# Kernel optimization log

Measured on AMD Instinct MI355X. Metric: run time of the kernel, lower is better.

The kernel has to match this reference:

```python
import jax, jax.numpy as jnp
import numpy as np

N = 10000      # nodes
E = 160000     # edges (avg degree 16)
D = 128        # channels
H = 4          # heads
C = 128        # per-head dim (PyG: out_channels per head = channels)
HC = H * C
EPS_SOFTMAX = 1e-16
EPS_NORM = 1e-5


def setup_inputs() -> dict:
    key = jax.random.key(0)
    ks = jax.random.split(key, 12)
    s = 1.0 / np.sqrt(D)
    sb = 1.0 / np.sqrt(3 * D)
    return {
        "x": jax.random.normal(ks[0], (N, D), jnp.float32),
        "edge_index": jax.random.randint(ks[1], (2, E), 0, N, dtype=jnp.int64),
        "Wq": jax.random.normal(ks[2], (D, HC), jnp.float32) * s,
        "bq": jnp.zeros((HC,), jnp.float32),
        "Wk": jax.random.normal(ks[3], (D, HC), jnp.float32) * s,
        "bk": jnp.zeros((HC,), jnp.float32),
        "Wv": jax.random.normal(ks[4], (D, HC), jnp.float32) * s,
        "bv": jnp.zeros((HC,), jnp.float32),
        "Wskip": jax.random.normal(ks[5], (D, D), jnp.float32) * s,
        "bskip": jnp.zeros((D,), jnp.float32),
        "Wbeta": jax.random.normal(ks[6], (3 * D,), jnp.float32) * sb,  # lin_beta, bias=False
        "gn_weight": jnp.ones((D,), jnp.float32),
        "gn_bias": jnp.zeros((D,), jnp.float32),
        "gn_mean_scale": jnp.ones((D,), jnp.float32),
    }


def reference(x, edge_index, Wq, bq, Wk, bk, Wv, bv, Wskip, bskip, Wbeta,
              gn_weight, gn_bias, gn_mean_scale):
    n = x.shape[0]
    src, dst = edge_index[0], edge_index[1]  # messages flow src(j) -> dst(i)

    # Projections [N,H,C]
    q = (x @ Wq + bq).reshape(n, H, C)
    k = (x @ Wk + bk).reshape(n, H, C)
    v = (x @ Wv + bv).reshape(n, H, C)

    # Per-edge attention logits [E,H]
    alpha = jnp.einsum('ehc,ehc->eh', q[dst], k[src]) / jnp.sqrt(jnp.float32(C))

    # Segment softmax over incoming edges of each dst node
    amax = jax.ops.segment_max(alpha, dst, num_segments=n)       # [N,H]
    amax = jnp.where(jnp.isfinite(amax), amax, 0.0)
    ex = jnp.exp(alpha - amax[dst])                              # [E,H]
    denom = jax.ops.segment_sum(ex, dst, num_segments=n)         # [N,H]
    attn = ex / (denom[dst] + EPS_SOFTMAX)                       # [E,H]

    # Weighted scatter-aggregate, then mean over heads (concat=False)
    msgs = attn[:, :, None] * v[src]                             # [E,H,C]
    out = jax.ops.segment_sum(msgs, dst, num_segments=n)         # [N,H,C]
    out = out.mean(axis=1)                                       # [N,D]

    # Beta-gated skip (PyG: beta = sigmoid(lin_beta([out, x_r, out - x_r])))
    skip = x @ Wskip + bskip
    beta = jax.nn.sigmoid(jnp.concatenate([out, skip, out - skip], axis=-1) @ Wbeta)
    beta = beta[:, None]
    out = beta * skip + (1.0 - beta) * out

    # GraphNorm (single graph): (x - mean_scale*mean) / sqrt(var + eps) * w + b
    mean = out.mean(axis=0)
    centered = out - gn_mean_scale * mean
    var = (centered * centered).mean(axis=0)
    out = gn_weight * centered / jnp.sqrt(var + EPS_NORM) + gn_bias

    # GELU (exact) + residual (shapes match); dropout is identity in eval
    out = jax.nn.gelu(out, approximate=False)
    return out + x
```

## Files before the change

kernel.cpp:

```cpp
#include <hip/hip_runtime.h>
#include <hip/hip_bf16.h>
#include <math.h>

#define D_DIM 128
#define HC_DIM 512
#define CAP 128

typedef __attribute__((ext_vector_type(8))) short bf16x8;
typedef __attribute__((ext_vector_type(4))) float f32x4;
typedef __attribute__((ext_vector_type(2))) float f32x2;
typedef __attribute__((ext_vector_type(2))) _Float16 h16x2;

static __device__ __forceinline__ unsigned short f2bf(float f) {
  unsigned u = __float_as_uint(f);
  unsigned r = (u + 0x7fffu + ((u >> 16) & 1u)) >> 16;
  return (unsigned short)r;
}
static __device__ __forceinline__ float bflo(unsigned u) {
  return __uint_as_float(u << 16);
}
static __device__ __forceinline__ float bfhi(unsigned u) {
  return __uint_as_float(u & 0xffff0000u);
}

__global__ void prep_kernel(const float* __restrict__ x,
                            const float* __restrict__ Wq, const float* __restrict__ Wk,
                            const float* __restrict__ Wv, const float* __restrict__ Wskip,
                            const float* __restrict__ bq, const float* __restrict__ bk,
                            const float* __restrict__ bv, const float* __restrict__ bskip,
                            unsigned short* __restrict__ xb,
                            unsigned short* __restrict__ wcat,
                            float* __restrict__ bcat,
                            int* __restrict__ zbase, int zwords, int N) {
  int t = blockIdx.x * 256 + threadIdx.x;
  int X4 = N * 32;
  if (t < X4) {
    float4 f = *(const float4*)&x[t * 4];
    ushort4 o;
    o.x = f2bf(f.x); o.y = f2bf(f.y); o.z = f2bf(f.z); o.w = f2bf(f.w);
    *(ushort4*)&xb[t * 4] = o;
  } else if (t < X4 + 1664 * 128) {
    int widx = t - X4;
    if (widx < 3 * 65536) {
      int segi = widx >> 16;
      int r = widx & 65535;
      int kk = r >> 9;
      int m = r & 511;
      const float* W = (segi == 0) ? Wq : (segi == 1) ? Wk : Wv;
      wcat[(size_t)(segi * 512 + m) * 128 + kk] = f2bf(W[kk * 512 + m]);
    } else {
      int r = widx - 3 * 65536;
      int kk = r >> 7;
      int m = r & 127;
      wcat[(size_t)(1536 + m) * 128 + kk] = f2bf(Wskip[kk * 128 + m]);
    }
  } else if (t < X4 + 1664 * 128 + 1664) {
    int b = t - X4 - 1664 * 128;
    bcat[b] = (b < 512) ? bq[b] : (b < 1024) ? bk[b - 512]
            : (b < 1536) ? bv[b - 1024] : bskip[b - 1536];
  } else if (t < X4 + 1664 * 128 + 1664 + zwords) {
    zbase[t - X4 - 1664 * 128 - 1664] = 0;
  }
}

__global__ __launch_bounds__(256) void gemm_mfma_kernel(
    const unsigned short* __restrict__ Xb, const unsigned short* __restrict__ Wt,
    const float* __restrict__ bcat, unsigned short* __restrict__ qb,
    unsigned short* __restrict__ kf, unsigned char* __restrict__ v8,
    float* __restrict__ skip,
    const int* __restrict__ src, const int* __restrict__ dst,
    int* __restrict__ cnt, int* __restrict__ bsrc, int N, int E) {
  const int tid = threadIdx.x;
  {
    int nblk = gridDim.x * gridDim.y;
    int lb = blockIdx.y * gridDim.x + blockIdx.x;
    int per = (E + nblk - 1) / nblk;
    int e0 = lb * per;
    int e1 = min(e0 + per, E);
    for (int e = e0 + tid; e < e1; e += 256) {
      int d = dst[e];
      int p = atomicAdd(&cnt[d], 1);
      if (p < CAP) bsrc[d * CAP + p] = src[e];
    }
  }
  const int wave = tid >> 6, lane = tid & 63;
  const int l16 = lane & 15, quad = lane >> 4;
  const int row0 = (blockIdx.x * 4 + wave) * 64;
  const int col0 = blockIdx.y * 64;

  const unsigned short* xrow[4];
#pragma unroll
  for (int i = 0; i < 4; ++i) {
    int r = row0 + i * 16 + l16;
    if (r >= N) r = N - 1;
    xrow[i] = Xb + (size_t)r * 128;
  }
  const unsigned short* wrow[4];
  float bias[4];
#pragma unroll
  for (int j = 0; j < 4; ++j) {
    int c = col0 + j * 16 + l16;
    wrow[j] = Wt + (size_t)c * 128;
    bias[j] = bcat[c];
  }

  f32x4 acc[4][4] = {};
#pragma unroll
  for (int kk = 0; kk < 4; ++kk) {
    int k0 = kk * 32 + quad * 8;
    bf16x8 a[4], b[4];
#pragma unroll
    for (int i = 0; i < 4; ++i) a[i] = *(const bf16x8*)(xrow[i] + k0);
#pragma unroll
    for (int j = 0; j < 4; ++j) b[j] = *(const bf16x8*)(wrow[j] + k0);
#pragma unroll
    for (int i = 0; i < 4; ++i)
#pragma unroll
      for (int j = 0; j < 4; ++j)
        acc[i][j] = __builtin_amdgcn_mfma_f32_16x16x32_bf16(a[i], b[j], acc[i][j], 0, 0, 0);
  }

  const int kind = (col0 < 512) ? 0 : (col0 < 1024) ? 1 : (col0 < 1536) ? 2 : 3;
#pragma unroll
  for (int i = 0; i < 4; ++i) {
#pragma unroll
    for (int reg = 0; reg < 4; ++reg) {
      int r = row0 + i * 16 + quad * 4 + reg;
      if (r < N) {
#pragma unroll
        for (int j = 0; j < 4; ++j) {
          int cidx = col0 + j * 16 + l16;
          float val = acc[i][j][reg] + bias[j];
          if (kind == 0) {
            qb[(size_t)r * 512 + cidx] = f2bf(val);
          } else if (kind == 1) {
            _Float16 hv = (_Float16)val;
            kf[(size_t)r * 512 + cidx - 512] = *(unsigned short*)&hv;
          } else if (kind == 2) {
            int pk = __builtin_amdgcn_cvt_pk_fp8_f32(val, val, 0, false);
            v8[(size_t)r * 512 + cidx - 1024] = (unsigned char)pk;
          } else {
            skip[(size_t)r * 128 + cidx - 1536] = val;
          }
        }
      }
    }
  }
}

__global__ __launch_bounds__(256) void attn_kernel(
    const unsigned short* __restrict__ qb, const unsigned short* __restrict__ kf,
    const unsigned char* __restrict__ v8, const int* __restrict__ cnt,
    const int* __restrict__ bsrc, unsigned* __restrict__ oh, int N, int nper) {
  int bx = blockIdx.x;
  int head = bx / nper;
  int tid = threadIdx.x;
  int w = tid >> 6, lane = tid & 63;
  int node = (bx - head * nper) * 4 + w;
  if (node >= N) return;
  int g = lane >> 4, j = lane & 15;

  const float qscale = 0.08838834764831845f * 1.4426950408889634f;
  int4 qi = *(const int4*)(qb + (size_t)node * 512 + head * 128 + j * 8);
  h16x2 qh0, qh1, qh2, qh3;
  qh0[0] = (_Float16)(bflo(qi.x) * qscale); qh0[1] = (_Float16)(bfhi(qi.x) * qscale);
  qh1[0] = (_Float16)(bflo(qi.y) * qscale); qh1[1] = (_Float16)(bfhi(qi.y) * qscale);
  qh2[0] = (_Float16)(bflo(qi.z) * qscale); qh2[1] = (_Float16)(bfhi(qi.z) * qscale);
  qh3[0] = (_Float16)(bflo(qi.w) * qscale); qh3[1] = (_Float16)(bfhi(qi.w) * qscale);

  const unsigned short* kb = kf + head * 128 + j * 8;
  const unsigned char* vb = v8 + head * 128 + j * 8;
  int count = min(cnt[node], CAP);
  const int* bp = bsrc + node * CAP;
  float lsum = 0.f;
  float o0 = 0.f, o1 = 0.f, o2 = 0.f, o3 = 0.f;
  float o4 = 0.f, o5 = 0.f, o6 = 0.f, o7 = 0.f;

  if (count > 0) {
    int e = bp[(g < count) ? g : 0];
    uint4 kw = *(const uint4*)(kb + (size_t)e * 512);
    uint2 vw = *(const uint2*)(vb + (size_t)e * 512);
    for (int idx = 0; idx < count; idx += 4) {
      int rem = count - idx;
      int nrem = rem - 4;
      int en = (nrem > 0) ? bp[idx + 4 + ((g < nrem) ? g : 0)] : e;
      uint4 kwn = *(const uint4*)(kb + (size_t)en * 512);
      uint2 vwn = *(const uint2*)(vb + (size_t)en * 512);
      float p = __builtin_amdgcn_fdot2(qh0, *(h16x2*)&kw.x, 0.f, false);
      p = __builtin_amdgcn_fdot2(qh1, *(h16x2*)&kw.y, p, false);
      p = __builtin_amdgcn_fdot2(qh2, *(h16x2*)&kw.z, p, false);
      p = __builtin_amdgcn_fdot2(qh3, *(h16x2*)&kw.w, p, false);
      p += __shfl_xor(p, 1);
      p += __shfl_xor(p, 2);
      p += __shfl_xor(p, 4);
      p += __shfl_xor(p, 8);
      float a = (g < rem) ? p : -1e30f;
      float wgt = exp2f(a);
      f32x2 v01 = __builtin_amdgcn_cvt_pk_f32_fp8(vw.x, false);
      f32x2 v23 = __builtin_amdgcn_cvt_pk_f32_fp8(vw.x, true);
      f32x2 v45 = __builtin_amdgcn_cvt_pk_f32_fp8(vw.y, false);
      f32x2 v67 = __builtin_amdgcn_cvt_pk_f32_fp8(vw.y, true);
      lsum += wgt;
      o0 += wgt * v01.x; o1 += wgt * v01.y;
      o2 += wgt * v23.x; o3 += wgt * v23.y;
      o4 += wgt * v45.x; o5 += wgt * v45.y;
      o6 += wgt * v67.x; o7 += wgt * v67.y;
      kw = kwn; vw = vwn; e = en;
    }
  }
  o0 += __shfl_xor(o0, 16); o0 += __shfl_xor(o0, 32);
  o1 += __shfl_xor(o1, 16); o1 += __shfl_xor(o1, 32);
  o2 += __shfl_xor(o2, 16); o2 += __shfl_xor(o2, 32);
  o3 += __shfl_xor(o3, 16); o3 += __shfl_xor(o3, 32);
  o4 += __shfl_xor(o4, 16); o4 += __shfl_xor(o4, 32);
  o5 += __shfl_xor(o5, 16); o5 += __shfl_xor(o5, 32);
  o6 += __shfl_xor(o6, 16); o6 += __shfl_xor(o6, 32);
  o7 += __shfl_xor(o7, 16); o7 += __shfl_xor(o7, 32);
  lsum += __shfl_xor(lsum, 16); lsum += __shfl_xor(lsum, 32);
  float inv = 1.f / (lsum + 1e-16f);
  if (g == 0) {
    unsigned d0 = (unsigned)f2bf(o0 * inv) | ((unsigned)f2bf(o1 * inv) << 16);
    unsigned d1 = (unsigned)f2bf(o2 * inv) | ((unsigned)f2bf(o3 * inv) << 16);
    unsigned d2 = (unsigned)f2bf(o4 * inv) | ((unsigned)f2bf(o5 * inv) << 16);
    unsigned d3 = (unsigned)f2bf(o6 * inv) | ((unsigned)f2bf(o7 * inv) << 16);
    int4 st; st.x = (int)d0; st.y = (int)d1; st.z = (int)d2; st.w = (int)d3;
    *(int4*)(oh + ((size_t)head * N + node) * 64 + j * 4) = st;
  }
}

__global__ __launch_bounds__(256) void combine_kernel(
    const unsigned* __restrict__ oh, const float* __restrict__ skip,
    const float* __restrict__ Wbeta, float* __restrict__ out2,
    float* __restrict__ colsum, float* __restrict__ colsq, int N) {
  int tid = threadIdx.x;
  int lane = tid & 63, w = tid >> 6;
  int wid = blockIdx.x * 4 + w;
  float2 wb0 = *(const float2*)&Wbeta[lane * 2];
  float2 wb1 = *(const float2*)&Wbeta[128 + lane * 2];
  float2 wb2 = *(const float2*)&Wbeta[256 + lane * 2];
  float cs0 = 0.f, cq0 = 0.f, cs1 = 0.f, cq1 = 0.f;
#pragma unroll
  for (int k = 0; k < 4; ++k) {
    int n = wid + k * 2500;
    if (n < N) {
      unsigned h0 = oh[((size_t)0 * N + n) * 64 + lane];
      unsigned h1 = oh[((size_t)1 * N + n) * 64 + lane];
      unsigned h2 = oh[((size_t)2 * N + n) * 64 + lane];
      unsigned h3 = oh[((size_t)3 * N + n) * 64 + lane];
      float a0 = 0.25f * (bflo(h0) + bflo(h1) + bflo(h2) + bflo(h3));
      float a1 = 0.25f * (bfhi(h0) + bfhi(h1) + bfhi(h2) + bfhi(h3));
      float2 s = *(const float2*)&skip[(size_t)n * 128 + lane * 2];
      float p = a0 * wb0.x + s.x * wb1.x + (a0 - s.x) * wb2.x +
                a1 * wb0.y + s.y * wb1.y + (a1 - s.y) * wb2.y;
#pragma unroll
      for (int dmask = 1; dmask < 64; dmask <<= 1) p += __shfl_xor(p, dmask);
      float beta = 1.f / (1.f + __expf(-p));
      float o0 = beta * s.x + (1.f - beta) * a0;
      float o1 = beta * s.y + (1.f - beta) * a1;
      float2 ov; ov.x = o0; ov.y = o1;
      *(float2*)&out2[(size_t)n * 128 + lane * 2] = ov;
      cs0 += o0; cq0 += o0 * o0;
      cs1 += o1; cq1 += o1 * o1;
    }
  }
  __shared__ float red[4][128];
  __shared__ float redq[4][128];
  red[w][lane * 2] = cs0;
  red[w][lane * 2 + 1] = cs1;
  redq[w][lane * 2] = cq0;
  redq[w][lane * 2 + 1] = cq1;
  __syncthreads();
  if (w == 0) {
    int c = lane * 2;
    float s0 = red[0][c] + red[1][c] + red[2][c] + red[3][c];
    float s1 = red[0][c + 1] + red[1][c + 1] + red[2][c + 1] + red[3][c + 1];
    float q0 = redq[0][c] + redq[1][c] + redq[2][c] + redq[3][c];
    float q1 = redq[0][c + 1] + redq[1][c + 1] + redq[2][c + 1] + redq[3][c + 1];
    atomicAdd(&colsum[c], s0);
    atomicAdd(&colsum[c + 1], s1);
    atomicAdd(&colsq[c], q0);
    atomicAdd(&colsq[c + 1], q1);
  }
}

__global__ void final_kernel(const float* __restrict__ out2,
                             const float* __restrict__ colsum,
                             const float* __restrict__ colsq,
                             const float* __restrict__ gnw,
                             const float* __restrict__ gnb,
                             const float* __restrict__ gnms,
                             const float* __restrict__ x,
                             float* __restrict__ y, int total2, float invN) {
  int i = blockIdx.x * 256 + threadIdx.x;
  if (i < total2) {
    int c = (i & 63) * 2;
    float2 cs = *(const float2*)&colsum[c];
    float2 cq = *(const float2*)&colsq[c];
    float2 gw = *(const float2*)&gnw[c];
    float2 gb = *(const float2*)&gnb[c];
    float2 gs = *(const float2*)&gnms[c];
    float mean0 = cs.x * invN, mean1 = cs.y * invN;
    float var0 = cq.x * invN - mean0 * mean0 * gs.x * (2.f - gs.x);
    float var1 = cq.y * invN - mean1 * mean1 * gs.y * (2.f - gs.y);
    float mul0 = gw.x / sqrtf(var0 + 1e-5f);
    float mul1 = gw.y / sqrtf(var1 + 1e-5f);
    float2 o = *(const float2*)&out2[i * 2];
    float2 xx = *(const float2*)&x[i * 2];
    float t0 = (o.x - gs.x * mean0) * mul0 + gb.x;
    float t1 = (o.y - gs.y * mean1) * mul1 + gb.y;
    float g0 = 0.5f * t0 * (1.f + erff(t0 * 0.70710678118654752f));
    float g1 = 0.5f * t1 * (1.f + erff(t1 * 0.70710678118654752f));
    float2 r; r.x = g0 + xx.x; r.y = g1 + xx.y;
    *(float2*)&y[i * 2] = r;
  }
}

extern "C" void kernel_launch(void* const* d_in, const int* in_sizes, int n_in,
                              void* d_out, int out_size, void* d_ws, size_t ws_size,
                              hipStream_t stream) {
  const float* x     = (const float*)d_in[0];
  const int*   ei    = (const int*)d_in[1];
  const float* Wq    = (const float*)d_in[2];
  const float* bq    = (const float*)d_in[3];
  const float* Wk    = (const float*)d_in[4];
  const float* bk    = (const float*)d_in[5];
  const float* Wv    = (const float*)d_in[6];
  const float* bv    = (const float*)d_in[7];
  const float* Wskip = (const float*)d_in[8];
  const float* bskip = (const float*)d_in[9];
  const float* Wbeta = (const float*)d_in[10];
  const float* gnw   = (const float*)d_in[11];
  const float* gnb   = (const float*)d_in[12];
  const float* gnms  = (const float*)d_in[13];

  const int N = in_sizes[0] / D_DIM;
  const int E = in_sizes[1] / 2;
  const int* src = ei;
  const int* dst = ei + E;

  char* p = (char*)d_ws;
  unsigned short* qb = (unsigned short*)p; p += (size_t)N * 512 * 2;
  unsigned short* kf = (unsigned short*)p; p += (size_t)N * 512 * 2;
  unsigned char*  v8 = (unsigned char*)p;  p += (size_t)N * 512;
  unsigned*       oh = (unsigned*)p;       p += (size_t)4 * N * 64 * 4;
  float*          skip = (float*)p;        p += (size_t)N * 128 * 4;
  float*          out2 = (float*)p;        p += (size_t)N * 128 * 4;
  int*   cnt    = (int*)p;   p += (size_t)N * 4;
  float* colsum = (float*)p; p += 128 * 4;
  float* colsq  = (float*)p; p += 128 * 4;
  int zwords = N + 256;
  int* bsrc   = (int*)p;   p += (size_t)N * CAP * 4;
  unsigned short* wcat = (unsigned short*)p; p += (size_t)1664 * 128 * 2;
  float* bcat = (float*)p; p += 1664 * 4;
  unsigned short* xb = (unsigned short*)oh;

  int prepTotal = N * 32 + 1664 * 128 + 1664 + zwords;
  prep_kernel<<<(prepTotal + 255) / 256, 256, 0, stream>>>(
      x, Wq, Wk, Wv, Wskip, bq, bk, bv, bskip, xb, wcat, bcat, cnt, zwords, N);

  gemm_mfma_kernel<<<dim3(40, 26), 256, 0, stream>>>(
      xb, wcat, bcat, qb, kf, v8, skip, src, dst, cnt, bsrc, N, E);

  int nper = (N + 3) / 4;
  attn_kernel<<<nper * 4, 256, 0, stream>>>(qb, kf, v8, cnt, bsrc, oh, N, nper);

  combine_kernel<<<625, 256, 0, stream>>>(oh, skip, Wbeta, out2, colsum, colsq, N);

  int total2 = N * D_DIM / 2;
  final_kernel<<<(total2 + 255) / 256, 256, 0, stream>>>(
      out2, colsum, colsq, gnw, gnb, gnms, x, (float*)d_out, total2, 1.f / (float)N);
}
```

Measured before the change: 192.9 us.

## Fuse attention and beta-gated combine into one kernel looping over heads

Merges the per-head attention kernel and the combine kernel into one kernel. Each wave handles one node, loops over all four heads, averages them in registers, then applies the beta gate and accumulates GraphNorm column statistics. This removes the bf16 per-head intermediate buffer, its write and re-read, and one kernel launch. Edge indices are staged in shared memory and reused across heads, and the column-sum atomics are spread over four replica slots that the final kernel adds back together. In exchange there are four times fewer blocks, each running a longer serial loop, which may reduce latency hiding for the gather loads.

Result: faster. 183.6 us (-4.8%).

```diff
diff --git a/kernel.cpp b/kernel.cpp
--- a/kernel.cpp
+++ b/kernel.cpp
@@ -5,6 +5,7 @@
 #define D_DIM 128
 #define HC_DIM 512
 #define CAP 128
+#define REP 4
 
 typedef __attribute__((ext_vector_type(8))) short bf16x8;
 typedef __attribute__((ext_vector_type(4))) float f32x4;
@@ -148,138 +149,147 @@
   }
 }
 
-__global__ __launch_bounds__(256) void attn_kernel(
+__global__ __launch_bounds__(256) void attn_combine_kernel(
     const unsigned short* __restrict__ qb, const unsigned short* __restrict__ kf,
     const unsigned char* __restrict__ v8, const int* __restrict__ cnt,
-    const int* __restrict__ bsrc, unsigned* __restrict__ oh, int N, int nper) {
-  int bx = blockIdx.x;
-  int head = bx / nper;
+    const int* __restrict__ bsrc, const float* __restrict__ skip,
+    const float* __restrict__ Wbeta, float* __restrict__ out2,
+    float* __restrict__ colsum, float* __restrict__ colsq, int N) {
+  __shared__ int eL[4][CAP];
+  __shared__ float redS[4][128];
+  __shared__ float redQ[4][128];
   int tid = threadIdx.x;
   int w = tid >> 6, lane = tid & 63;
-  int node = (bx - head * nper) * 4 + w;
-  if (node >= N) return;
+  int node = blockIdx.x * 4 + w;
+  bool nv = node < N;
+  int nc = nv ? node : (N - 1);
   int g = lane >> 4, j = lane & 15;
 
+  int count = nv ? min(cnt[nc], CAP) : 0;
+  const int* bp = bsrc + (size_t)nc * CAP;
+  for (int i = lane; i < count; i += 64) eL[w][i] = bp[i];
+
   const float qscale = 0.08838834764831845f * 1.4426950408889634f;
-  int4 qi = *(const int4*)(qb + (size_t)node * 512 + head * 128 + j * 8);
-  h16x2 qh0, qh1, qh2, qh3;
-  qh0[0] = (_Float16)(bflo(qi.x) * qscale); qh0[1] = (_Float16)(bfhi(qi.x) * qscale);
-  qh1[0] = (_Float16)(bflo(qi.y) * qscale); qh1[1] = (_Float16)(bfhi(qi.y) * qscale);
-  qh2[0] = (_Float16)(bflo(qi.z) * qscale); qh2[1] = (_Float16)(bfhi(qi.z) * qscale);
-  qh3[0] = (_Float16)(bflo(qi.w) * qscale); qh3[1] = (_Float16)(bfhi(qi.w) * qscale);
-
-  const unsigned short* kb = kf + head * 128 + j * 8;
-  const unsigned char* vb = v8 + head * 128 + j * 8;
-  int count = min(cnt[node], CAP);
-  const int* bp = bsrc + node * CAP;
-  float lsum = 0.f;
-  float o0 = 0.f, o1 = 0.f, o2 = 0.f, o3 = 0.f;
-  float o4 = 0.f, o5 = 0.f, o6 = 0.f, o7 = 0.f;
-
-  if (count > 0) {
-    int e = bp[(g < count) ? g : 0];
-    uint4 kw = *(const uint4*)(kb + (size_t)e * 512);
-    uint2 vw = *(const uint2*)(vb + (size_t)e * 512);
-    for (int idx = 0; idx < count; idx += 4) {
-      int rem = count - idx;
-      int nrem = rem - 4;
-      int en = (nrem > 0) ? bp[idx + 4 + ((g < nrem) ? g : 0)] : e;
-      uint4 kwn = *(const uint4*)(kb + (size_t)en * 512);
-      uint2 vwn = *(const uint2*)(vb + (size_t)en * 512);
-      float p = __builtin_amdgcn_fdot2(qh0, *(h16x2*)&kw.x, 0.f, false);
-      p = __builtin_amdgcn_fdot2(qh1, *(h16x2*)&kw.y, p, false);
-      p = __builtin_amdgcn_fdot2(qh2, *(h16x2*)&kw.z, p, false);
-      p = __builtin_amdgcn_fdot2(qh3, *(h16x2*)&kw.w, p, false);
-      p += __shfl_xor(p, 1);
-      p += __shfl_xor(p, 2);
-      p += __shfl_xor(p, 4);
-      p += __shfl_xor(p, 8);
-      float a = (g < rem) ? p : -1e30f;
-      float wgt = exp2f(a);
-      f32x2 v01 = __builtin_amdgcn_cvt_pk_f32_fp8(vw.x, false);
-      f32x2 v23 = __builtin_amdgcn_cvt_pk_f32_fp8(vw.x, true);
-      f32x2 v45 = __builtin_amdgcn_cvt_pk_f32_fp8(vw.y, false);
-      f32x2 v67 = __builtin_amdgcn_cvt_pk_f32_fp8(vw.y, true);
-      lsum += wgt;
-      o0 += wgt * v01.x; o1 += wgt * v01.y;
-      o2 += wgt * v23.x; o3 += wgt * v23.y;
-      o4 += wgt * v45.x; o5 += wgt * v45.y;
-      o6 += wgt * v67.x; o7 += wgt * v67.y;
-      kw = kwn; vw = vwn; e = en;
-    }
-  }
-  o0 += __shfl_xor(o0, 16); o0 += __shfl_xor(o0, 32);
-  o1 += __shfl_xor(o1, 16); o1 += __shfl_xor(o1, 32);
-  o2 += __shfl_xor(o2, 16); o2 += __shfl_xor(o2, 32);
-  o3 += __shfl_xor(o3, 16); o3 += __shfl_xor(o3, 32);
-  o4 += __shfl_xor(o4, 16); o4 += __shfl_xor(o4, 32);
-  o5 += __shfl_xor(o5, 16); o5 += __shfl_xor(o5, 32);
-  o6 += __shfl_xor(o6, 16); o6 += __shfl_xor(o6, 32);
-  o7 += __shfl_xor(o7, 16); o7 += __shfl_xor(o7, 32);
-  lsum += __shfl_xor(lsum, 16); lsum += __shfl_xor(lsum, 32);
-  float inv = 1.f / (lsum + 1e-16f);
+  float am0 = 0.f, am1 = 0.f, am2 = 0.f, am3 = 0.f;
+  float am4 = 0.f, am5 = 0.f, am6 = 0.f, am7 = 0.f;
+
+#pragma unroll 1
+  for (int h = 0; h < 4; ++h) {
+    int4 qi = *(const int4*)(qb + (size_t)nc * 512 + h * 128 + j * 8);
+    h16x2 qh0, qh1, qh2, qh3;
+    qh0[0] = (_Float16)(bflo(qi.x) * qscale); qh0[1] = (_Float16)(bfhi(qi.x) * qscale);
+    qh1[0] = (_Float16)(bflo(qi.y) * qscale); qh1[1] = (_Float16)(bfhi(qi.y) * qscale);
+    qh2[0] = (_Float16)(bflo(qi.z) * qscale); qh2[1] = (_Float16)(bfhi(qi.z) * qscale);
+    qh3[0] = (_Float16)(bflo(qi.w) * qscale); qh3[1] = (_Float16)(bfhi(qi.w) * qscale);
+
+    const unsigned short* kb = kf + h * 128 + j * 8;
+    const unsigned char* vb = v8 + h * 128 + j * 8;
+    float lsum = 0.f;
+    float o0 = 0.f, o1 = 0.f, o2 = 0.f, o3 = 0.f;
+    float o4 = 0.f, o5 = 0.f, o6 = 0.f, o7 = 0.f;
+
+    if (count > 0) {
+      int e = eL[w][(g < count) ? g : 0];
+      uint4 kw = *(const uint4*)(kb + (size_t)e * 512);
+      uint2 vw = *(const uint2*)(vb + (size_t)e * 512);
+      for (int idx = 0; idx < count; idx += 4) {
+        int rem = count - idx;
+        int nrem = rem - 4;
+        int en = (nrem > 0) ? eL[w][idx + 4 + ((g < nrem) ? g : 0)] : e;
+        uint4 kwn = *(const uint4*)(kb + (size_t)en * 512);
+        uint2 vwn = *(const uint2*)(vb + (size_t)en * 512);
+        float p = __builtin_amdgcn_fdot2(qh0, *(h16x2*)&kw.x, 0.f, false);
+        p = __builtin_amdgcn_fdot2(qh1, *(h16x2*)&kw.y, p, false);
+        p = __builtin_amdgcn_fdot2(qh2, *(h16x2*)&kw.z, p, false);
+        p = __builtin_amdgcn_fdot2(qh3, *(h16x2*)&kw.w, p, false);
+        p += __shfl_xor(p, 1);
+        p += __shfl_xor(p, 2);
+        p += __shfl_xor(p, 4);
+        p += __shfl_xor(p, 8);
+        float a = (g < rem) ? p : -1e30f;
+        float wgt = exp2f(a);
+        f32x2 v01 = __builtin_amdgcn_cvt_pk_f32_fp8(vw.x, false);
+        f32x2 v23 = __builtin_amdgcn_cvt_pk_f32_fp8(vw.x, true);
+        f32x2 v45 = __builtin_amdgcn_cvt_pk_f32_fp8(vw.y, false);
+        f32x2 v67 = __builtin_amdgcn_cvt_pk_f32_fp8(vw.y, true);
+        lsum += wgt;
+        o0 += wgt * v01.x; o1 += wgt * v01.y;
+        o2 += wgt * v23.x; o3 += wgt * v23.y;
+        o4 += wgt * v45.x; o5 += wgt * v45.y;
+        o6 += wgt * v67.x; o7 += wgt * v67.y;
+        kw = kwn; vw = vwn; e = en;
+      }
+    }
+    o0 += __shfl_xor(o0, 16); o0 += __shfl_xor(o0, 32);
+    o1 += __shfl_xor(o1, 16); o1 += __shfl_xor(o1, 32);
+    o2 += __shfl_xor(o2, 16); o2 += __shfl_xor(o2, 32);
+    o3 += __shfl_xor(o3, 16); o3 += __shfl_xor(o3, 32);
+    o4 += __shfl_xor(o4, 16); o4 += __shfl_xor(o4, 32);
+    o5 += __shfl_xor(o5, 16); o5 += __shfl_xor(o5, 32);
+    o6 += __shfl_xor(o6, 16); o6 += __shfl_xor(o6, 32);
+    o7 += __shfl_xor(o7, 16); o7 += __shfl_xor(o7, 32);
+    lsum += __shfl_xor(lsum, 16); lsum += __shfl_xor(lsum, 32);
+    float inv = 0.25f / (lsum + 1e-16f);
+    am0 += o0 * inv; am1 += o1 * inv; am2 += o2 * inv; am3 += o3 * inv;
+    am4 += o4 * inv; am5 += o5 * inv; am6 += o6 * inv; am7 += o7 * inv;
+  }
+
+  float4 sl = *(const float4*)&skip[(size_t)nc * 128 + j * 8];
+  float4 sh = *(const float4*)&skip[(size_t)nc * 128 + j * 8 + 4];
+  float4 wal = *(const float4*)&Wbeta[j * 8];
+  float4 wah = *(const float4*)&Wbeta[j * 8 + 4];
+  float4 wbl = *(const float4*)&Wbeta[128 + j * 8];
+  float4 wbh = *(const float4*)&Wbeta[128 + j * 8 + 4];
+  float4 wcl = *(const float4*)&Wbeta[256 + j * 8];
+  float4 wch = *(const float4*)&Wbeta[256 + j * 8 + 4];
+  float p = am0 * wal.x + sl.x * wbl.x + (am0 - sl.x) * wcl.x
+          + am1 * wal.y + sl.y * wbl.y + (am1 - sl.y) * wcl.y
+          + am2 * wal.z + sl.z * wbl.z + (am2 - sl.z) * wcl.z
+          + am3 * wal.w + sl.w * wbl.w + (am3 - sl.w) * wcl.w
+          + am4 * wah.x + sh.x * wbh.x + (am4 - sh.x) * wch.x
+          + am5 * wah.y + sh.y * wbh.y + (am5 - sh.y) * wch.y
+          + am6 * wah.z + sh.z * wbh.z + (am6 - sh.z) * wch.z
+          + am7 * wah.w + sh.w * wbh.w + (am7 - sh.w) * wch.w;
+  p += __shfl_xor(p, 1); p += __shfl_xor(p, 2);
+  p += __shfl_xor(p, 4); p += __shfl_xor(p, 8);
+  float beta = 1.f / (1.f + __expf(-p));
+  float ob = 1.f - beta;
+  float vm = nv ? 1.f : 0.f;
+  float oc0 = (beta * sl.x + ob * am0) * vm;
+  float oc1 = (beta * sl.y + ob * am1) * vm;
+  float oc2 = (beta * sl.z + ob * am2) * vm;
+  float oc3 = (beta * sl.w + ob * am3) * vm;
+  float oc4 = (beta * sh.x + ob * am4) * vm;
+  float oc5 = (beta * sh.y + ob * am5) * vm;
+  float oc6 = (beta * sh.z + ob * am6) * vm;
+  float oc7 = (beta * sh.w + ob * am7) * vm;
+
   if (g == 0) {
-    unsigned d0 = (unsigned)f2bf(o0 * inv) | ((unsigned)f2bf(o1 * inv) << 16);
-    unsigned d1 = (unsigned)f2bf(o2 * inv) | ((unsigned)f2bf(o3 * inv) << 16);
-    unsigned d2 = (unsigned)f2bf(o4 * inv) | ((unsigned)f2bf(o5 * inv) << 16);
-    unsigned d3 = (unsigned)f2bf(o6 * inv) | ((unsigned)f2bf(o7 * inv) << 16);
-    int4 st; st.x = (int)d0; st.y = (int)d1; st.z = (int)d2; st.w = (int)d3;
-    *(int4*)(oh + ((size_t)head * N + node) * 64 + j * 4) = st;
-  }
-}
-
-__global__ __launch_bounds__(256) void combine_kernel(
-    const unsigned* __restrict__ oh, const float* __restrict__ skip,
-    const float* __restrict__ Wbeta, float* __restrict__ out2,
-    float* __restrict__ colsum, float* __restrict__ colsq, int N) {
-  int tid = threadIdx.x;
-  int lane = tid & 63, w = tid >> 6;
-  int wid = blockIdx.x * 4 + w;
-  float2 wb0 = *(const float2*)&Wbeta[lane * 2];
-  float2 wb1 = *(const float2*)&Wbeta[128 + lane * 2];
-  float2 wb2 = *(const float2*)&Wbeta[256 + lane * 2];
-  float cs0 = 0.f, cq0 = 0.f, cs1 = 0.f, cq1 = 0.f;
-#pragma unroll
-  for (int k = 0; k < 4; ++k) {
-    int n = wid + k * 2500;
-    if (n < N) {
-      unsigned h0 = oh[((size_t)0 * N + n) * 64 + lane];
-      unsigned h1 = oh[((size_t)1 * N + n) * 64 + lane];
-      unsigned h2 = oh[((size_t)2 * N + n) * 64 + lane];
-      unsigned h3 = oh[((size_t)3 * N + n) * 64 + lane];
-      float a0 = 0.25f * (bflo(h0) + bflo(h1) + bflo(h2) + bflo(h3));
-      float a1 = 0.25f * (bfhi(h0) + bfhi(h1) + bfhi(h2) + bfhi(h3));
-      float2 s = *(const float2*)&skip[(size_t)n * 128 + lane * 2];
-      float p = a0 * wb0.x + s.x * wb1.x + (a0 - s.x) * wb2.x +
-                a1 * wb0.y + s.y * wb1.y + (a1 - s.y) * wb2.y;
-#pragma unroll
-      for (int dmask = 1; dmask < 64; dmask <<= 1) p += __shfl_xor(p, dmask);
-      float beta = 1.f / (1.f + __expf(-p));
-      float o0 = beta * s.x + (1.f - beta) * a0;
-      float o1 = beta * s.y + (1.f - beta) * a1;
-      float2 ov; ov.x = o0; ov.y = o1;
-      *(float2*)&out2[(size_t)n * 128 + lane * 2] = ov;
-      cs0 += o0; cq0 += o0 * o0;
-      cs1 += o1; cq1 += o1 * o1;
-    }
-  }
-  __shared__ float red[4][128];
-  __shared__ float redq[4][128];
-  red[w][lane * 2] = cs0;
-  red[w][lane * 2 + 1] = cs1;
-  redq[w][lane * 2] = cq0;
-  redq[w][lane * 2 + 1] = cq1;
+    float4 lo; lo.x = oc0; lo.y = oc1; lo.z = oc2; lo.w = oc3;
+    float4 hi; hi.x = oc4; hi.y = oc5; hi.z = oc6; hi.w = oc7;
+    if (nv) {
+      *(float4*)&out2[(size_t)node * 128 + j * 8] = lo;
+      *(float4*)&out2[(size_t)node * 128 + j * 8 + 4] = hi;
+    }
+    *(float4*)&redS[w][j * 8] = lo;
+    *(float4*)&redS[w][j * 8 + 4] = hi;
+    float4 ql; ql.x = oc0 * oc0; ql.y = oc1 * oc1; ql.z = oc2 * oc2; ql.w = oc3 * oc3;
+    float4 qh; qh.x = oc4 * oc4; qh.y = oc5 * oc5; qh.z = oc6 * oc6; qh.w = oc7 * oc7;
+    *(float4*)&redQ[w][j * 8] = ql;
+    *(float4*)&redQ[w][j * 8 + 4] = qh;
+  }
   __syncthreads();
   if (w == 0) {
     int c = lane * 2;
-    float s0 = red[0][c] + red[1][c] + red[2][c] + red[3][c];
-    float s1 = red[0][c + 1] + red[1][c + 1] + red[2][c + 1] + red[3][c + 1];
-    float q0 = redq[0][c] + redq[1][c] + redq[2][c] + redq[3][c];
-    float q1 = redq[0][c + 1] + redq[1][c + 1] + redq[2][c + 1] + redq[3][c + 1];
-    atomicAdd(&colsum[c], s0);
-    atomicAdd(&colsum[c + 1], s1);
-    atomicAdd(&colsq[c], q0);
-    atomicAdd(&colsq[c + 1], q1);
+    float s0 = redS[0][c] + redS[1][c] + redS[2][c] + redS[3][c];
+    float s1 = redS[0][c + 1] + redS[1][c + 1] + redS[2][c + 1] + redS[3][c + 1];
+    float q0 = redQ[0][c] + redQ[1][c] + redQ[2][c] + redQ[3][c];
+    float q1 = redQ[0][c + 1] + redQ[1][c + 1] + redQ[2][c + 1] + redQ[3][c + 1];
+    int slot = (blockIdx.x & (REP - 1)) * 128;
+    atomicAdd(&colsum[slot + c], s0);
+    atomicAdd(&colsum[slot + c + 1], s1);
+    atomicAdd(&colsq[slot + c], q0);
+    atomicAdd(&colsq[slot + c + 1], q1);
   }
 }
 
@@ -294,8 +304,15 @@
   int i = blockIdx.x * 256 + threadIdx.x;
   if (i < total2) {
     int c = (i & 63) * 2;
-    float2 cs = *(const float2*)&colsum[c];
-    float2 cq = *(const float2*)&colsq[c];
+    float2 cs; cs.x = 0.f; cs.y = 0.f;
+    float2 cq; cq.x = 0.f; cq.y = 0.f;
+#pragma unroll
+    for (int s = 0; s < REP; ++s) {
+      float2 t = *(const float2*)&colsum[s * 128 + c];
+      float2 u = *(const float2*)&colsq[s * 128 + c];
+      cs.x += t.x; cs.y += t.y;
+      cq.x += u.x; cq.y += u.y;
+    }
     float2 gw = *(const float2*)&gnw[c];
     float2 gb = *(const float2*)&gnb[c];
     float2 gs = *(const float2*)&gnms[c];
@@ -342,17 +359,16 @@
   unsigned short* qb = (unsigned short*)p; p += (size_t)N * 512 * 2;
   unsigned short* kf = (unsigned short*)p; p += (size_t)N * 512 * 2;
   unsigned char*  v8 = (unsigned char*)p;  p += (size_t)N * 512;
-  unsigned*       oh = (unsigned*)p;       p += (size_t)4 * N * 64 * 4;
   float*          skip = (float*)p;        p += (size_t)N * 128 * 4;
   float*          out2 = (float*)p;        p += (size_t)N * 128 * 4;
   int*   cnt    = (int*)p;   p += (size_t)N * 4;
-  float* colsum = (float*)p; p += 128 * 4;
-  float* colsq  = (float*)p; p += 128 * 4;
-  int zwords = N + 256;
+  float* colsum = (float*)p; p += REP * 128 * 4;
+  float* colsq  = (float*)p; p += REP * 128 * 4;
+  int zwords = N + 2 * REP * 128;
   int* bsrc   = (int*)p;   p += (size_t)N * CAP * 4;
   unsigned short* wcat = (unsigned short*)p; p += (size_t)1664 * 128 * 2;
   float* bcat = (float*)p; p += 1664 * 4;
-  unsigned short* xb = (unsigned short*)oh;
+  unsigned short* xb = (unsigned short*)out2;
 
   int prepTotal = N * 32 + 1664 * 128 + 1664 + zwords;
   prep_kernel<<<(prepTotal + 255) / 256, 256, 0, stream>>>(
@@ -361,10 +377,8 @@
   gemm_mfma_kernel<<<dim3(40, 26), 256, 0, stream>>>(
       xb, wcat, bcat, qb, kf, v8, skip, src, dst, cnt, bsrc, N, E);
 
-  int nper = (N + 3) / 4;
-  attn_kernel<<<nper * 4, 256, 0, stream>>>(qb, kf, v8, cnt, bsrc, oh, N, nper);
-
-  combine_kernel<<<625, 256, 0, stream>>>(oh, skip, Wbeta, out2, colsum, colsq, N);
+  attn_combine_kernel<<<(N + 3) / 4, 256, 0, stream>>>(
+      qb, kf, v8, cnt, bsrc, skip, Wbeta, out2, colsum, colsq, N);
 
   int total2 = N * D_DIM / 2;
   final_kernel<<<(total2 + 255) / 256, 256, 0, stream>>>(
```
